# Kernel optimization log

Hardware: AMD Instinct MI355X
Metric: run time of the kernel (lower is better)

The kernel has to match this reference:

```python
import jax, jax.numpy as jnp
import numpy as np

NUM_FEATURES = 4
LATENT = 16
HIDDEN = 128
N_PIECES = 20
B, P = 8192, 128


def setup_inputs() -> dict:
    key = jax.random.key(0)
    ks = jax.random.split(key, 8)
    s = lambda fan_in: 1.0 / np.sqrt(fan_in)
    return {
        "x": jax.random.normal(ks[0], (B, P * NUM_FEATURES), jnp.float32),
        "W1": jax.random.normal(ks[1], (NUM_FEATURES, HIDDEN), jnp.float32) * s(NUM_FEATURES),
        "b1": jnp.zeros((HIDDEN,), jnp.float32),
        "W2": jax.random.normal(ks[2], (HIDDEN, HIDDEN), jnp.float32) * s(HIDDEN),
        "b2": jnp.zeros((HIDDEN,), jnp.float32),
        "W3": jax.random.normal(ks[3], (HIDDEN, 2 * LATENT), jnp.float32) * s(HIDDEN),
        "b3": jnp.zeros((2 * LATENT,), jnp.float32),
        "pool_weight": jax.random.normal(ks[4], (2 * LATENT, N_PIECES + 1), jnp.float32) * 0.1,
        "eps": jax.random.normal(ks[5], (B, LATENT), jnp.float32),
    }


def _fspool_weights(pool_weight, set_size):
    # piecewise-linear interpolation of pool_weight over normalized rank positions
    pos = jnp.arange(set_size, dtype=jnp.float32) / (set_size - 1) * N_PIECES  # [P]
    idx = jnp.clip(pos.astype(jnp.int32), 0, N_PIECES)
    frac = pos - idx.astype(jnp.float32)
    left = pool_weight[:, idx]                                   # [C, P]
    right = pool_weight[:, jnp.clip(idx + 1, 0, N_PIECES)]       # [C, P]
    return (1.0 - frac) * left + frac * right                    # [C, P]


def reference(x, W1, b1, W2, b2, W3, b3, pool_weight, eps):
    # per-particle shared MLP, batched over particles (B, P, F) -> (B, P, 2L)
    h = x.reshape(B, P, NUM_FEATURES)
    h = jax.nn.relu(jnp.einsum("bpf,fh->bph", h, W1) + b1)
    h = jax.nn.relu(jnp.einsum("bph,hk->bpk", h, W2) + b2)
    h = jnp.einsum("bph,hc->bpc", h, W3) + b3                    # [B, P, 2L]
    z = jnp.transpose(h, (0, 2, 1))                              # [B, 2L, P]
    # FSPool: descending featurewise sort + rank-weighted sum over set dim
    z_sorted = jnp.flip(jnp.sort(z, axis=-1), axis=-1)           # [B, 2L, P]
    w = _fspool_weights(pool_weight, P)                          # [2L, P]
    pooled = jnp.sum(z_sorted * w[None], axis=-1)                # [B, 2L]
    mus = pooled[:, ::2]
    logvars = pooled[:, 1::2]
    samples = mus + eps * jnp.exp(0.5 * logvars)
    return (mus, logvars, samples)
```

## Files before the change

### kernel.cpp

```cpp
#include <hip/hip_runtime.h>

#define B_TOT 8192
#define NB    16
#define NPCS  20

typedef __attribute__((ext_vector_type(8))) __fp16 f16x8;
typedef __attribute__((ext_vector_type(4))) float f32x4;
typedef __attribute__((ext_vector_type(2))) __fp16 fp16x2;

__device__ __forceinline__ unsigned pkmax(unsigned a, unsigned b) {
    unsigned d; asm("v_pk_max_f16 %0, %1, %2" : "=v"(d) : "v"(a), "v"(b)); return d;
}
__device__ __forceinline__ unsigned pkmin(unsigned a, unsigned b) {
    unsigned d; asm("v_pk_min_f16 %0, %1, %2" : "=v"(d) : "v"(a), "v"(b)); return d;
}
__device__ __forceinline__ unsigned pkrne(float a, float b) {
    fp16x2 h;
    h.x = (__fp16)a;
    h.y = (__fp16)b;
    return __builtin_bit_cast(unsigned, h);
}
__device__ __forceinline__ unsigned pkrtz(float a, float b) {
    return __builtin_bit_cast(unsigned, __builtin_amdgcn_cvt_pkrtz(a, b));
}
__device__ __forceinline__ float asf(unsigned u) { return __builtin_bit_cast(float, u); }
__device__ __forceinline__ unsigned asu(float f) { return __builtin_bit_cast(unsigned, f); }
__device__ __forceinline__ fp16x2 ash2(unsigned u) { return __builtin_bit_cast(fp16x2, u); }
__device__ __forceinline__ unsigned asu2(fp16x2 h) { return __builtin_bit_cast(unsigned, h); }

template<int CTRL>
__device__ __forceinline__ unsigned dppmov(unsigned v) {
    return (unsigned)__builtin_amdgcn_mov_dpp((int)v, CTRL, 0xf, 0xf, true);
}
__device__ __forceinline__ unsigned xlane(unsigned v, int lm) {
    switch (lm) {
    case 1:  return dppmov<0xB1>(v);
    case 2:  return dppmov<0x4E>(v);
    case 4:  return (unsigned)__builtin_amdgcn_ds_swizzle((int)v, 0x101F);
    default: return dppmov<0x128>(v);
    }
}
__device__ __forceinline__ float xlanef(float v, int lm) { return asf(xlane(asu(v), lm)); }

#define WS_W3T 32768
#define WS_WSP 40960
#define WS_W1D 57344
#define WS_B1D 59392

__device__ __forceinline__ unsigned dup16(float f) {
    unsigned short u = __builtin_bit_cast(unsigned short, (__fp16)f);
    return (unsigned)u * 0x10001u;
}

__global__ void prep_kernel(const float* __restrict__ W1, const float* __restrict__ b1,
                            const float* __restrict__ W2, const float* __restrict__ W3,
                            const float* __restrict__ pw, void* __restrict__ ws)
{
    const int t = blockIdx.x * 256 + threadIdx.x;
    __fp16* w2t = (__fp16*)ws;
    __fp16* w3t = (__fp16*)((char*)ws + WS_W3T);
    float* wsp  = (float*)((char*)ws + WS_WSP);
    unsigned* w1d = (unsigned*)((char*)ws + WS_W1D);
    unsigned* b1d = (unsigned*)((char*)ws + WS_B1D);
    if (t < 16384) {
        int j = t >> 7, k = t & 127;
        w2t[t] = (__fp16)W2[k * 128 + j];
    } else if (t < 20480) {
        int o = t - 16384, c = o >> 7, k = o & 127;
        w3t[o] = (__fp16)W3[k * 32 + c];
    } else if (t < 24576) {
        int o = t - 20480, c = o >> 7, p = o & 127;
        float pos = (float)p * (20.0f / 127.0f);
        int ip = min((int)pos, NPCS);
        float fr = pos - (float)ip;
        int ipb = min(ip + 1, NPCS);
        wsp[o] = (1.0f - fr) * pw[c * 21 + ip] + fr * pw[c * 21 + ipb];
    } else if (t < 24704) {
        int h = t - 24576;
        w1d[h * 4 + 0] = dup16(W1[h]);
        w1d[h * 4 + 1] = dup16(W1[128 + h]);
        w1d[h * 4 + 2] = dup16(W1[256 + h]);
        w1d[h * 4 + 3] = dup16(W1[384 + h]);
        b1d[h] = dup16(b1[h]);
    }
}

#define L_SCRT 32768
#define L_SZP  49152
#define L_W1D  57600
#define L_B1D  59648
#define L_POOL 60160

__global__ __launch_bounds__(256, 2) void enc_kernel(
    const float* __restrict__ x,   const float* __restrict__ b1g,
    const float* __restrict__ b2g, const float* __restrict__ b3g,
    const float* __restrict__ eps, const void* __restrict__ ws,
    float* __restrict__ out)
{
    __shared__ __align__(16) char smem[62208];

    const int tid  = threadIdx.x;
    const int wv   = tid >> 6;
    const int lane = tid & 63;
    const int l16  = lane & 15;
    const int quad = lane >> 4;
    const int b0   = blockIdx.x * NB;

    {
        const uint4* src = (const uint4*)ws;
#pragma unroll
        for (int it = 0; it < 8; ++it) {
            int idx = tid + it * 256;
            int j = idx >> 4, ch = idx & 15;
            *(uint4*)(smem + j * 256 + ((ch ^ (j & 15)) * 16)) = src[idx];
        }
    }
    if (tid < 160) ((uint4*)(smem + L_W1D))[tid] = ((const uint4*)((const char*)ws + WS_W1D))[tid];

    f16x8 w3f[2][4];
    {
        const __fp16* w3t = (const __fp16*)((const char*)ws + WS_W3T);
#pragma unroll
        for (int mt2 = 0; mt2 < 2; ++mt2)
#pragma unroll
            for (int kt = 0; kt < 4; ++kt)
                w3f[mt2][kt] = *(const f16x8*)(w3t + (mt2 * 16 + l16) * 128 + kt * 32 + quad * 8);
    }
    f32x4 b3acc[2];
    {
        float4 t0 = *(const float4*)(b3g + quad * 4);
        float4 t1 = *(const float4*)(b3g + 16 + quad * 4);
        b3acc[0] = (f32x4){t0.x, t0.y, t0.z, t0.w};
        b3acc[1] = (f32x4){t1.x, t1.y, t1.z, t1.w};
    }
    f32x4 b2acc[8];
#pragma unroll
    for (int nt = 0; nt < 8; ++nt) {
        const float bv = b2g[nt * 16 + l16];
        b2acc[nt] = (f32x4){bv, bv, bv, bv};
    }

    const int pr = wv * 4 + quad;
    float wE[8], wO[8];
    {
        const float* wsp = (const float*)((const char*)ws + WS_WSP);
        float4 e0 = *(const float4*)(wsp + (2 * pr) * 128 + l16 * 8);
        float4 e1 = *(const float4*)(wsp + (2 * pr) * 128 + l16 * 8 + 4);
        float4 o0 = *(const float4*)(wsp + (2 * pr + 1) * 128 + l16 * 8);
        float4 o1 = *(const float4*)(wsp + (2 * pr + 1) * 128 + l16 * 8 + 4);
        wE[0]=e0.x; wE[1]=e0.y; wE[2]=e0.z; wE[3]=e0.w; wE[4]=e1.x; wE[5]=e1.y; wE[6]=e1.z; wE[7]=e1.w;
        wO[0]=o0.x; wO[1]=o0.y; wO[2]=o0.z; wO[3]=o0.w; wO[4]=o1.x; wO[5]=o1.y; wO[6]=o1.z; wO[7]=o1.w;
    }

    const int ib = l16 * 8;
    const unsigned sfl8  = (ib & 8)  ? 0x80008000u : 0u;
    const unsigned sfl16 = (ib & 16) ? 0x80008000u : 0u;
    const unsigned sfl32 = (ib & 32) ? 0x80008000u : 0u;
    const unsigned sfl64 = (ib & 64) ? 0x80008000u : 0u;

    __syncthreads();

    char*     scrTw = (char*)(smem + L_SCRT + wv * 4096);
    unsigned* szp   = (unsigned*)(smem + L_SZP);
    float*    spool = (float*)(smem + L_POOL);

    const float* xptr = x + (size_t)b0 * 512 + (wv * 32 + l16) * 4;
    float4 xv0 = *(const float4*)(xptr);
    float4 xv1 = *(const float4*)(xptr + 64);

    for (int e = 0; e < NB; ++e) {
        const unsigned xp0 = pkrtz(xv0.x, xv1.x);
        const unsigned xp1 = pkrtz(xv0.y, xv1.y);
        const unsigned xp2 = pkrtz(xv0.z, xv1.z);
        const unsigned xp3 = pkrtz(xv0.w, xv1.w);

        if (e + 1 < NB) {
            xv0 = *(const float4*)(xptr + (e + 1) * 512);
            xv1 = *(const float4*)(xptr + (e + 1) * 512 + 64);
        }

        union AF { unsigned u[4]; f16x8 v; } a1[2][4];
#pragma unroll
        for (int kt = 0; kt < 4; ++kt) {
            const int k8 = kt * 32 + quad * 8;
#pragma unroll
            for (int jp = 0; jp < 4; ++jp) {
                const int h = k8 + 2 * jp;
                const uint4 wa = *(const uint4*)(smem + L_W1D + h * 16);
                const uint4 wb = *(const uint4*)(smem + L_W1D + h * 16 + 16);
                const uint2 bp = *(const uint2*)(smem + L_B1D + h * 4);
                fp16x2 accA = ash2(bp.x);
                fp16x2 accB = ash2(bp.y);
                accA = __builtin_elementwise_fma(ash2(xp0), ash2(wa.x), accA);
                accA = __builtin_elementwise_fma(ash2(xp1), ash2(wa.y), accA);
                accA = __builtin_elementwise_fma(ash2(xp2), ash2(wa.z), accA);
                accA = __builtin_elementwise_fma(ash2(xp3), ash2(wa.w), accA);
                accB = __builtin_elementwise_fma(ash2(xp0), ash2(wb.x), accB);
                accB = __builtin_elementwise_fma(ash2(xp1), ash2(wb.y), accB);
                accB = __builtin_elementwise_fma(ash2(xp2), ash2(wb.z), accB);
                accB = __builtin_elementwise_fma(ash2(xp3), ash2(wb.w), accB);
                const unsigned uA = pkmax(asu2(accA), 0u);
                const unsigned uB = pkmax(asu2(accB), 0u);
                a1[0][kt].u[jp] = __builtin_amdgcn_perm(uA, uB, 0x01000504u);
                a1[1][kt].u[jp] = __builtin_amdgcn_perm(uA, uB, 0x03020706u);
            }
        }

        f32x4 acc2[2][8];
#pragma unroll
        for (int kt = 0; kt < 4; ++kt)
#pragma unroll
            for (int nt = 0; nt < 8; ++nt) {
                const int j = nt * 16 + l16;
                const int phys = (kt * 4 + quad) ^ l16;
                f16x8 bf = *(const f16x8*)(smem + j * 256 + phys * 16);
                if (kt == 0) {
                    acc2[0][nt] = __builtin_amdgcn_mfma_f32_16x16x32_f16(a1[0][0].v, bf, b2acc[nt], 0, 0, 0);
                    acc2[1][nt] = __builtin_amdgcn_mfma_f32_16x16x32_f16(a1[1][0].v, bf, b2acc[nt], 0, 0, 0);
                } else {
                    acc2[0][nt] = __builtin_amdgcn_mfma_f32_16x16x32_f16(a1[0][kt].v, bf, acc2[0][nt], 0, 0, 0);
                    acc2[1][nt] = __builtin_amdgcn_mfma_f32_16x16x32_f16(a1[1][kt].v, bf, acc2[1][nt], 0, 0, 0);
                }
            }

#pragma unroll
        for (int mt = 0; mt < 2; ++mt) {
#pragma unroll
            for (int nt = 0; nt < 8; ++nt) {
                const int h = nt * 16 + l16;
                uint2 pk;
                pk.x = pkmax(pkrtz(acc2[mt][nt][0], acc2[mt][nt][1]), 0u);
                pk.y = pkmax(pkrtz(acc2[mt][nt][2], acc2[mt][nt][3]), 0u);
                *(uint2*)(scrTw + (h >> 2) * 128 + (h & 3) * 32 + quad * 8) = pk;
            }
            asm volatile("s_waitcnt lgkmcnt(0)" ::: "memory");

            union A3 { __fp16 h[8]; f16x8 v; } a3[4];
            {
                const __fp16* rbase = (const __fp16*)(scrTw + quad * 256) + l16;
#pragma unroll
                for (int kt = 0; kt < 4; ++kt) {
                    const __fp16* rp = rbase + kt * 512;
#pragma unroll
                    for (int j = 0; j < 8; ++j)
                        a3[kt].h[j] = rp[j * 16];
                }
            }

            const int colbase = wv * 32 + mt * 16;
#pragma unroll
            for (int mt2 = 0; mt2 < 2; ++mt2) {
                f32x4 acc = __builtin_amdgcn_mfma_f32_16x16x32_f16(w3f[mt2][0], a3[0].v, b3acc[mt2], 0, 0, 0);
#pragma unroll
                for (int kt = 1; kt < 4; ++kt)
                    acc = __builtin_amdgcn_mfma_f32_16x16x32_f16(w3f[mt2][kt], a3[kt].v, acc, 0, 0, 0);
                const int prw = 8 * mt2 + 2 * quad;
                szp[prw * 132 + colbase + l16]       = pkrne(acc[0], acc[1]);
                szp[(prw + 1) * 132 + colbase + l16] = pkrne(acc[2], acc[3]);
            }
            asm volatile("" ::: "memory");
        }
        __syncthreads();

        unsigned v[8];
        {
            const unsigned* zp = szp + pr * 132 + l16 * 8;
            uint4 za = *(const uint4*)zp;
            uint4 zb = *(const uint4*)(zp + 4);
            v[0]=za.x; v[1]=za.y; v[2]=za.z; v[3]=za.w;
            v[4]=zb.x; v[5]=zb.y; v[6]=zb.z; v[7]=zb.w;
        }
#pragma unroll
        for (int k = 2; k <= 128; k <<= 1) {
#pragma unroll
            for (int j = 64; j >= 1; j >>= 1) {
                if (j >= k) continue;
                if (j >= 8) {
                    const bool km = ((ib & k) == 0) != ((ib & j) != 0);
                    const int lm = j >> 3;
#pragma unroll
                    for (int r = 0; r < 8; ++r) {
                        unsigned p = xlane(v[r], lm);
                        unsigned mx = pkmax(v[r], p), mn = pkmin(v[r], p);
                        v[r] = km ? mx : mn;
                    }
                } else if (k <= 4) {
#pragma unroll
                    for (int a = 0; a < 8; ++a) {
                        if (a & j) continue;
                        const int bx = a | j;
                        unsigned mx = pkmax(v[a], v[bx]), mn = pkmin(v[a], v[bx]);
                        if ((a & k) == 0) { v[a] = mx; v[bx] = mn; }
                        else              { v[a] = mn; v[bx] = mx; }
                    }
                } else {
                    const unsigned sfl = (k == 8) ? sfl8 : (k == 16) ? sfl16 :
                                         (k == 32) ? sfl32 : (k == 64) ? sfl64 : 0u;
                    if (j == 4 && k != 128) {
#pragma unroll
                        for (int r = 0; r < 8; ++r) v[r] ^= sfl;
                    }
#pragma unroll
                    for (int a = 0; a < 8; ++a) {
                        if (a & j) continue;
                        const int bx = a | j;
                        unsigned mx = pkmax(v[a], v[bx]), mn = pkmin(v[a], v[bx]);
                        v[a] = mx; v[bx] = mn;
                    }
                    if (j == 1 && k != 128) {
#pragma unroll
                        for (int r = 0; r < 8; ++r) v[r] ^= sfl;
                    }
                }
            }
        }

        float sE = 0.f, sO = 0.f;
#pragma unroll
        for (int r = 0; r < 8; ++r) {
            const fp16x2 hv = ash2(v[r]);
            sE = fmaf(wE[r], (float)hv.x, sE);
            sO = fmaf(wO[r], (float)hv.y, sO);
        }
#pragma unroll
        for (int d = 8; d >= 1; d >>= 1) {
            sE += xlanef(sE, d);
            sO += xlanef(sO, d);
        }
        if (l16 == 0) {
            spool[e * 32 + 2 * pr]     = sE;
            spool[e * 32 + 2 * pr + 1] = sO;
        }
        __syncthreads();
    }

    {
        const int e = tid >> 4, t = tid & 15;
        const float mu = spool[e * 32 + 2 * t];
        const float lv = spool[e * 32 + 2 * t + 1];
        const float ev = eps[(size_t)b0 * 16 + tid];
        const float smp = fmaf(ev, __expf(0.5f * lv), mu);
        out[(size_t)b0 * 16 + tid] = mu;
        out[(size_t)B_TOT * 16 + (size_t)b0 * 16 + tid] = lv;
        out[(size_t)2 * B_TOT * 16 + (size_t)b0 * 16 + tid] = smp;
    }
}

extern "C" void kernel_launch(void* const* d_in, const int* in_sizes, int n_in,
                              void* d_out, int out_size, void* d_ws, size_t ws_size,
                              hipStream_t stream) {
    const float* x   = (const float*)d_in[0];
    const float* W1  = (const float*)d_in[1];
    const float* b1  = (const float*)d_in[2];
    const float* W2  = (const float*)d_in[3];
    const float* b2  = (const float*)d_in[4];
    const float* W3  = (const float*)d_in[5];
    const float* b3  = (const float*)d_in[6];
    const float* pw  = (const float*)d_in[7];
    const float* eps = (const float*)d_in[8];
    float* out = (float*)d_out;

    prep_kernel<<<dim3(97), dim3(256), 0, stream>>>(W1, b1, W2, W3, pw, d_ws);
    enc_kernel<<<dim3(B_TOT / NB), dim3(256), 0, stream>>>(x, b1, b2, b3, eps, d_ws, out);
}
```

Before: 180.8 us.

## Swap MFMA operands and permute W2 to drop LDS transpose between layers

The layer-2 MFMA now takes weights as the A operand and activations as B, and W2 columns are permuted in prep so the output registers already match the layer-3 operand layout. This removes the per-wave LDS scratch transpose with its strided half-word reads and wait. The freed LDS lets occupancy rise from 2 to 3 blocks per CU, and fewer elements per block (NB 16 to 8) doubles the grid. The b2 bias load is adjusted to the new output layout. Smaller blocks mean more per-block setup overhead relative to useful work.

```diff
diff --git a/kernel.cpp b/kernel.cpp
--- a/kernel.cpp
+++ b/kernel.cpp
@@ -1,7 +1,7 @@
 #include <hip/hip_runtime.h>
 
 #define B_TOT 8192
-#define NB    16
+#define NB    8
 #define NPCS  20
 
 typedef __attribute__((ext_vector_type(8))) __fp16 f16x8;
@@ -50,6 +50,10 @@
 __device__ __forceinline__ unsigned dup16(float f) {
     unsigned short u = __builtin_bit_cast(unsigned short, (__fp16)f);
     return (unsigned)u * 0x10001u;
+}
+
+__device__ __forceinline__ int piperm(int j) {
+    return (j & 0x60) | ((j & 0x0C) << 1) | ((j & 0x10) >> 2) | (j & 3);
 }
 
 __global__ void prep_kernel(const float* __restrict__ W1, const float* __restrict__ b1,
@@ -64,7 +68,7 @@
     unsigned* b1d = (unsigned*)((char*)ws + WS_B1D);
     if (t < 16384) {
         int j = t >> 7, k = t & 127;
-        w2t[t] = (__fp16)W2[k * 128 + j];
+        w2t[t] = (__fp16)W2[k * 128 + piperm(j)];
     } else if (t < 20480) {
         int o = t - 16384, c = o >> 7, k = o & 127;
         w3t[o] = (__fp16)W3[k * 32 + c];
@@ -85,19 +89,18 @@
     }
 }
 
-#define L_SCRT 32768
-#define L_SZP  49152
-#define L_W1D  57600
-#define L_B1D  59648
-#define L_POOL 60160
-
-__global__ __launch_bounds__(256, 2) void enc_kernel(
+#define L_SZP  32768
+#define L_W1D  41216
+#define L_B1D  43264
+#define L_POOL 43776
+
+__global__ __launch_bounds__(256, 3) void enc_kernel(
     const float* __restrict__ x,   const float* __restrict__ b1g,
     const float* __restrict__ b2g, const float* __restrict__ b3g,
     const float* __restrict__ eps, const void* __restrict__ ws,
     float* __restrict__ out)
 {
-    __shared__ __align__(16) char smem[62208];
+    __shared__ __align__(16) char smem[44800];
 
     const int tid  = threadIdx.x;
     const int wv   = tid >> 6;
@@ -136,8 +139,8 @@
     f32x4 b2acc[8];
 #pragma unroll
     for (int nt = 0; nt < 8; ++nt) {
-        const float bv = b2g[nt * 16 + l16];
-        b2acc[nt] = (f32x4){bv, bv, bv, bv};
+        float4 t4 = *(const float4*)(b2g + (nt >> 1) * 32 + quad * 8 + (nt & 1) * 4);
+        b2acc[nt] = (f32x4){t4.x, t4.y, t4.z, t4.w};
     }
 
     const int pr = wv * 4 + quad;
@@ -160,7 +163,6 @@
 
     __syncthreads();
 
-    char*     scrTw = (char*)(smem + L_SCRT + wv * 4096);
     unsigned* szp   = (unsigned*)(smem + L_SZP);
     float*    spool = (float*)(smem + L_POOL);
 
@@ -213,38 +215,31 @@
             for (int nt = 0; nt < 8; ++nt) {
                 const int j = nt * 16 + l16;
                 const int phys = (kt * 4 + quad) ^ l16;
-                f16x8 bf = *(const f16x8*)(smem + j * 256 + phys * 16);
+                f16x8 wf = *(const f16x8*)(smem + j * 256 + phys * 16);
                 if (kt == 0) {
-                    acc2[0][nt] = __builtin_amdgcn_mfma_f32_16x16x32_f16(a1[0][0].v, bf, b2acc[nt], 0, 0, 0);
-                    acc2[1][nt] = __builtin_amdgcn_mfma_f32_16x16x32_f16(a1[1][0].v, bf, b2acc[nt], 0, 0, 0);
+                    acc2[0][nt] = __builtin_amdgcn_mfma_f32_16x16x32_f16(wf, a1[0][0].v, b2acc[nt], 0, 0, 0);
+                    acc2[1][nt] = __builtin_amdgcn_mfma_f32_16x16x32_f16(wf, a1[1][0].v, b2acc[nt], 0, 0, 0);
                 } else {
-                    acc2[0][nt] = __builtin_amdgcn_mfma_f32_16x16x32_f16(a1[0][kt].v, bf, acc2[0][nt], 0, 0, 0);
-                    acc2[1][nt] = __builtin_amdgcn_mfma_f32_16x16x32_f16(a1[1][kt].v, bf, acc2[1][nt], 0, 0, 0);
+                    acc2[0][nt] = __builtin_amdgcn_mfma_f32_16x16x32_f16(wf, a1[0][kt].v, acc2[0][nt], 0, 0, 0);
+                    acc2[1][nt] = __builtin_amdgcn_mfma_f32_16x16x32_f16(wf, a1[1][kt].v, acc2[1][nt], 0, 0, 0);
                 }
             }
 
 #pragma unroll
         for (int mt = 0; mt < 2; ++mt) {
+            unsigned pkx[8], pky[8];
 #pragma unroll
             for (int nt = 0; nt < 8; ++nt) {
-                const int h = nt * 16 + l16;
-                uint2 pk;
-                pk.x = pkmax(pkrtz(acc2[mt][nt][0], acc2[mt][nt][1]), 0u);
-                pk.y = pkmax(pkrtz(acc2[mt][nt][2], acc2[mt][nt][3]), 0u);
-                *(uint2*)(scrTw + (h >> 2) * 128 + (h & 3) * 32 + quad * 8) = pk;
-            }
-            asm volatile("s_waitcnt lgkmcnt(0)" ::: "memory");
-
-            union A3 { __fp16 h[8]; f16x8 v; } a3[4];
-            {
-                const __fp16* rbase = (const __fp16*)(scrTw + quad * 256) + l16;
-#pragma unroll
-                for (int kt = 0; kt < 4; ++kt) {
-                    const __fp16* rp = rbase + kt * 512;
-#pragma unroll
-                    for (int j = 0; j < 8; ++j)
-                        a3[kt].h[j] = rp[j * 16];
-                }
+                pkx[nt] = pkmax(pkrtz(acc2[mt][nt][0], acc2[mt][nt][1]), 0u);
+                pky[nt] = pkmax(pkrtz(acc2[mt][nt][2], acc2[mt][nt][3]), 0u);
+            }
+            union A3 { unsigned u[4]; f16x8 v; } a3[4];
+#pragma unroll
+            for (int kt = 0; kt < 4; ++kt) {
+                a3[kt].u[0] = pkx[2 * kt];
+                a3[kt].u[1] = pky[2 * kt];
+                a3[kt].u[2] = pkx[2 * kt + 1];
+                a3[kt].u[3] = pky[2 * kt + 1];
             }
 
             const int colbase = wv * 32 + mt * 16;
@@ -258,7 +253,6 @@
                 szp[prw * 132 + colbase + l16]       = pkrne(acc[0], acc[1]);
                 szp[(prw + 1) * 132 + colbase + l16] = pkrne(acc[2], acc[3]);
             }
-            asm volatile("" ::: "memory");
         }
         __syncthreads();
 
@@ -334,7 +328,7 @@
         __syncthreads();
     }
 
-    {
+    if (tid < NB * 16) {
         const int e = tid >> 4, t = tid & 15;
         const float mu = spool[e * 32 + 2 * t];
         const float lv = spool[e * 32 + 2 * t + 1];
```

Measured after the change: 260.0 us. 1.44x slower.
